# Optimization experiments

Measured on AMD Instinct MI355X. Metric: run time of the kernel, lower is better.

## Reference

```python
import jax, jax.numpy as jnp
import numpy as np

WL = 8  # word length passed to block_quantize_nearest


def block_quantize_nearest(x, wl=WL):
    """QPyTorch block_quantize_nearest with dim=0.

    One shared exponent per row (block = row of x.view(N, -1)).
    Equivalent math to the CUDA kernel: base exponent e = floor(log2(max|row|)),
    quantization step = 2^(e + 2 - wl), round-half-up in the rebased bit space.
    """
    flat = x.reshape(x.shape[0], -1)
    max_abs = jnp.max(jnp.abs(flat), axis=1, keepdims=True)  # [N, 1]
    tiny = jnp.asarray(np.finfo(np.float32).tiny, x.dtype)
    exp = jnp.floor(jnp.log2(jnp.maximum(max_abs, tiny)))
    step = jnp.exp2(exp + 2.0 - wl)                          # [N, 1]
    q = jnp.floor(flat / step + 0.5) * step                  # round-half-up
    q = jnp.where(max_abs > 0, q, flat)                      # all-zero rows pass through
    return q.reshape(x.shape)


def setup_inputs() -> dict:
    key = jax.random.key(0)
    k1, k2, k3 = jax.random.split(key, 3)
    B, D_IN, D_OUT = 8192, 4096, 4096
    x = jax.random.normal(k1, (B, D_IN), dtype=jnp.float32)
    # nn.Linear init scale ~ 1/sqrt(fan_in)
    W = jax.random.normal(k2, (D_OUT, D_IN), dtype=jnp.float32) * (1.0 / np.sqrt(D_IN))
    b = jax.random.normal(k3, (D_OUT,), dtype=jnp.float32) * (1.0 / np.sqrt(D_IN))
    return {"x": x, "W": W, "b": b}


def reference(x, W, b):
    # Linear: y = x @ W^T + b  (x already 2D, flatten(1) is identity)
    h = jnp.einsum('bi,oi->bo', x.reshape(x.shape[0], -1), W) + b
    q = block_quantize_nearest(h, WL)
    return jax.nn.relu(q)
```

## Files before the change

kernel.cpp:

```cpp
#include <hip/hip_runtime.h>

#define M 8192
#define N 4096
#define K 4096
#define BM 256
#define BN 256
#define BK 64
#define NKT (K / BK)
#define NIT (NKT / 2)

typedef __attribute__((ext_vector_type(8))) short bf16x8;
typedef __attribute__((ext_vector_type(4))) float f32x4;
typedef __attribute__((address_space(1))) const unsigned GU;
typedef __attribute__((address_space(3))) unsigned LU;

__device__ __forceinline__ unsigned short f2bf(float f) {
    unsigned u = __float_as_uint(f);
    u += 0x7fffu + ((u >> 16) & 1u);
    return (unsigned short)(u >> 16);
}

__global__ __launch_bounds__(256) void cvt_bf16(const float* __restrict__ src,
                                                unsigned short* __restrict__ dst,
                                                int n8) {
    const int stride = gridDim.x * blockDim.x;
    for (int i = blockIdx.x * blockDim.x + threadIdx.x; i < n8; i += stride) {
        f32x4 a = ((const f32x4*)src)[2 * i];
        f32x4 b = ((const f32x4*)src)[2 * i + 1];
        bf16x8 v;
        #pragma unroll
        for (int j = 0; j < 4; ++j) {
            v[j]     = (short)f2bf(a[j]);
            v[4 + j] = (short)f2bf(b[j]);
        }
        ((bf16x8*)dst)[i] = v;
    }
}

#define BAR()   __builtin_amdgcn_s_barrier()
#define LGKM0() do { asm volatile("s_waitcnt lgkmcnt(0)" ::: "memory"); \
                     __builtin_amdgcn_sched_barrier(0); } while (0)
#define LGKM8() asm volatile("s_waitcnt lgkmcnt(8)" ::: "memory")
#define VM6()   asm volatile("s_waitcnt vmcnt(6)" ::: "memory")

#define QUAD(AR, BR, MOFF, NOFF)                                               \
    do {                                                                       \
        __builtin_amdgcn_s_setprio(1);                                         \
        _Pragma("unroll")                                                      \
        for (int m_ = 0; m_ < 4; ++m_) {                                       \
            _Pragma("unroll")                                                  \
            for (int n_ = 0; n_ < 2; ++n_) {                                   \
                acc[MOFF + m_][NOFF + n_] =                                    \
                    __builtin_amdgcn_mfma_f32_16x16x32_bf16(                   \
                        AR[m_][0], BR[n_][0], acc[MOFF + m_][NOFF + n_], 0, 0, 0); \
                acc[MOFF + m_][NOFF + n_] =                                    \
                    __builtin_amdgcn_mfma_f32_16x16x32_bf16(                   \
                        AR[m_][1], BR[n_][1], acc[MOFF + m_][NOFF + n_], 0, 0, 0); \
            }                                                                  \
        }                                                                      \
        __builtin_amdgcn_s_setprio(0);                                         \
    } while (0)

__global__ __launch_bounds__(512, 2) void gemm_bf16(
    const unsigned short* __restrict__ xb, const unsigned short* __restrict__ wb,
    const float* __restrict__ bias, float* __restrict__ out,
    int* __restrict__ rowmax)
{
    __shared__ short As[2][16384];
    __shared__ short Bs[2][16384];

    const int bid = blockIdx.x;
    const int tm = bid % (M / BM);
    const int tn = bid / (M / BM);
    const int bm = tm * BM, bn = tn * BN;

    const int t    = threadIdx.x;
    const int w_id = t >> 6;
    const int l    = t & 63;
    const int wr   = w_id >> 2;
    const int wc   = w_id & 3;
    const int lr   = l & 15;
    const int g    = l >> 4;

    const int srow_l = l >> 2;
    const int scol_l = ((l & 3) * 8) ^ ((l >> 5) * 16);
    const int loff = lr * 32 + ((g * 8) ^ ((lr >> 3) << 4));

    auto stageA = [&](int buf, int h, int kt) {
        #pragma unroll
        for (int j = 0; j < 2; ++j) {
            const int s = w_id * 2 + j;
            const unsigned short* gp =
                xb + (size_t)(bm + h * 128 + (s >> 1) * 16 + srow_l) * K
                   + kt * 64 + (s & 1) * 32 + scol_l;
            __builtin_amdgcn_global_load_lds(
                (const GU*)gp, (LU*)&As[buf][h * 8192 + s * 512], 16, 0, 0);
        }
    };
    auto stageB = [&](int buf, int h, int kt) {
        #pragma unroll
        for (int j = 0; j < 2; ++j) {
            const int s = w_id * 2 + j;
            const unsigned short* gp =
                wb + (size_t)(bn + h * 128 + (s >> 1) * 16 + srow_l) * K
                   + kt * 64 + (s & 1) * 32 + scol_l;
            __builtin_amdgcn_global_load_lds(
                (const GU*)gp, (LU*)&Bs[buf][h * 8192 + s * 512], 16, 0, 0);
        }
    };
    auto ldA = [&](int buf, int m, int ks) -> bf16x8 {
        return *(const bf16x8*)&As[buf][wr * 8192 + (m * 2 + ks) * 512 + loff];
    };
    auto ldB = [&](int buf, int n, int ks) -> bf16x8 {
        return *(const bf16x8*)&Bs[buf][(wc >> 1) * 8192 +
                                        (((wc & 1) * 4 + n) * 2 + ks) * 512 + loff];
    };

    f32x4 acc[8][4];
    #pragma unroll
    for (int m = 0; m < 8; ++m)
        #pragma unroll
        for (int n = 0; n < 4; ++n)
            acc[m][n] = (f32x4){0.f, 0.f, 0.f, 0.f};

    bf16x8 a03[4][2], a47[4][2], b01[2][2], b23[2][2];

    stageB(0, 0, 0); stageB(0, 1, 0); stageA(0, 0, 0); stageA(0, 1, 0);
    stageB(1, 0, 1); stageB(1, 1, 1); stageA(1, 0, 1);
    VM6();
    BAR();

    for (int it = 0; it < NIT; ++it) {
        const int t1  = 2 * it + 1;
        const int tp0 = (2 * it + 2) & (NKT - 1);
        const int tp1 = (2 * it + 3) & (NKT - 1);

        #pragma unroll
        for (int m = 0; m < 4; ++m) { a03[m][0] = ldA(0, m, 0); a03[m][1] = ldA(0, m, 1); }
        #pragma unroll
        for (int n = 0; n < 2; ++n) { b01[n][0] = ldB(0, n, 0); b01[n][1] = ldB(0, n, 1); }
        stageA(1, 1, t1);
        LGKM8();
        BAR(); LGKM0();
        QUAD(a03, b01, 0, 0);
        BAR();

        #pragma unroll
        for (int n = 0; n < 2; ++n) { b23[n][0] = ldB(0, 2 + n, 0); b23[n][1] = ldB(0, 2 + n, 1); }
        stageB(0, 0, tp0);
        BAR(); LGKM0();
        QUAD(a03, b23, 0, 2);
        BAR();

        #pragma unroll
        for (int m = 0; m < 4; ++m) { a47[m][0] = ldA(0, 4 + m, 0); a47[m][1] = ldA(0, 4 + m, 1); }
        stageB(0, 1, tp0);
        BAR(); LGKM0();
        QUAD(a47, b23, 4, 2);
        BAR();

        stageA(0, 0, tp0);
        BAR(); LGKM0();
        QUAD(a47, b01, 4, 0);
        VM6();
        BAR();

        #pragma unroll
        for (int m = 0; m < 4; ++m) { a03[m][0] = ldA(1, m, 0); a03[m][1] = ldA(1, m, 1); }
        #pragma unroll
        for (int n = 0; n < 2; ++n) { b01[n][0] = ldB(1, n, 0); b01[n][1] = ldB(1, n, 1); }
        stageA(0, 1, tp0);
        LGKM8();
        BAR(); LGKM0();
        QUAD(a03, b01, 0, 0);
        BAR();

        #pragma unroll
        for (int n = 0; n < 2; ++n) { b23[n][0] = ldB(1, 2 + n, 0); b23[n][1] = ldB(1, 2 + n, 1); }
        stageB(1, 0, tp1);
        BAR(); LGKM0();
        QUAD(a03, b23, 0, 2);
        BAR();

        #pragma unroll
        for (int m = 0; m < 4; ++m) { a47[m][0] = ldA(1, 4 + m, 0); a47[m][1] = ldA(1, 4 + m, 1); }
        stageB(1, 1, tp1);
        BAR(); LGKM0();
        QUAD(a47, b23, 4, 2);
        BAR();

        stageA(1, 0, tp1);
        BAR(); LGKM0();
        QUAD(a47, b01, 4, 0);
        VM6();
        BAR();
    }

    float bv[4];
    #pragma unroll
    for (int n = 0; n < 4; ++n)
        bv[n] = bias[bn + wc * 64 + n * 16 + lr];

    #pragma unroll
    for (int m = 0; m < 8; ++m) {
        #pragma unroll
        for (int r = 0; r < 4; ++r) {
            const int row = bm + wr * 128 + m * 16 + g * 4 + r;
            float amax = 0.f;
            #pragma unroll
            for (int n = 0; n < 4; ++n) {
                const float v = acc[m][n][r] + bv[n];
                out[(size_t)row * N + (bn + wc * 64 + n * 16 + lr)] = v;
                amax = fmaxf(amax, fabsf(v));
            }
            #pragma unroll
            for (int off = 1; off < 16; off <<= 1)
                amax = fmaxf(amax, __shfl_xor(amax, off));
            if (lr == 0)
                atomicMax(rowmax + row, __float_as_int(amax));
        }
    }
}

__global__ __launch_bounds__(256) void quant_relu(
    float* __restrict__ y, const int* __restrict__ rowmax)
{
    const int nvec = (M * N) / 4;
    for (int i = blockIdx.x * blockDim.x + threadIdx.x; i < nvec;
         i += gridDim.x * blockDim.x) {
        const int row = i >> 10;
        const float mx = __int_as_float(rowmax[row]);
        f32x4 v = ((const f32x4*)y)[i];
        if (mx > 0.f) {
            const int e = ilogbf(mx);
            const float step = ldexpf(1.0f, e - 6);
            const float inv  = ldexpf(1.0f, 6 - e);
            #pragma unroll
            for (int j = 0; j < 4; ++j)
                v[j] = floorf(v[j] * inv + 0.5f) * step;
        }
        #pragma unroll
        for (int j = 0; j < 4; ++j)
            v[j] = fmaxf(v[j], 0.f);
        ((f32x4*)y)[i] = v;
    }
}

extern "C" void kernel_launch(void* const* d_in, const int* in_sizes, int n_in,
                              void* d_out, int out_size, void* d_ws, size_t ws_size,
                              hipStream_t stream) {
    const float* x = (const float*)d_in[0];
    const float* w = (const float*)d_in[1];
    const float* b = (const float*)d_in[2];
    float* out = (float*)d_out;

    const size_t XB = (size_t)M * K * 2;
    const size_t WB = (size_t)N * K * 2;

    unsigned short* xb = (unsigned short*)d_ws;
    unsigned short* wb = (unsigned short*)((char*)d_ws + XB);
    int* rowmax        = (int*)((char*)d_ws + XB + WB);

    hipMemsetAsync(rowmax, 0, M * sizeof(int), stream);
    cvt_bf16<<<2048, 256, 0, stream>>>(x, xb, (M * K) / 8);
    cvt_bf16<<<1024, 256, 0, stream>>>(w, wb, (N * K) / 8);
    gemm_bf16<<<dim3((M / BM) * (N / BN)), 512, 0, stream>>>(xb, wb, b, out, rowmax);
    quant_relu<<<2048, 256, 0, stream>>>(out, rowmax);
}
```

Baseline: 546.0 us.

## Stage GEMM epilogue through LDS for coalesced stores and fuse cvt kernels

The GEMM epilogue now writes the biased accumulators into the reused LDS buffer, one 128-row half at a time, and then issues fully coalesced 16-byte row-contiguous stores to the output. Previously each lane wrote scattered 4-byte values. The two bf16 conversion launches are also merged into one kernel that processes 4 elements per thread, saving one launch. The cost is extra barriers and an LDS round trip in the epilogue, and the conversion kernel now does narrower per-thread work.

Measured after the change: 534.9 us. 2.0% less time.

```diff
diff --git a/kernel.cpp b/kernel.cpp
--- a/kernel.cpp
+++ b/kernel.cpp
@@ -10,6 +10,7 @@
 #define NIT (NKT / 2)
 
 typedef __attribute__((ext_vector_type(8))) short bf16x8;
+typedef __attribute__((ext_vector_type(4))) short bf16x4;
 typedef __attribute__((ext_vector_type(4))) float f32x4;
 typedef __attribute__((address_space(1))) const unsigned GU;
 typedef __attribute__((address_space(3))) unsigned LU;
@@ -20,20 +21,23 @@
     return (unsigned short)(u >> 16);
 }
 
-__global__ __launch_bounds__(256) void cvt_bf16(const float* __restrict__ src,
-                                                unsigned short* __restrict__ dst,
-                                                int n8) {
+__global__ __launch_bounds__(256) void cvt_bf16_2(
+    const float* __restrict__ s1, unsigned short* __restrict__ d1, int n1_4,
+    const float* __restrict__ s2, unsigned short* __restrict__ d2, int n2_4)
+{
     const int stride = gridDim.x * blockDim.x;
-    for (int i = blockIdx.x * blockDim.x + threadIdx.x; i < n8; i += stride) {
-        f32x4 a = ((const f32x4*)src)[2 * i];
-        f32x4 b = ((const f32x4*)src)[2 * i + 1];
-        bf16x8 v;
-        #pragma unroll
-        for (int j = 0; j < 4; ++j) {
-            v[j]     = (short)f2bf(a[j]);
-            v[4 + j] = (short)f2bf(b[j]);
-        }
-        ((bf16x8*)dst)[i] = v;
+    const int total = n1_4 + n2_4;
+    for (int i = blockIdx.x * blockDim.x + threadIdx.x; i < total; i += stride) {
+        const float* s;
+        unsigned short* d;
+        int j;
+        if (i < n1_4) { s = s1; d = d1; j = i; }
+        else          { s = s2; d = d2; j = i - n1_4; }
+        f32x4 v = ((const f32x4*)s)[j];
+        bf16x4 o;
+        #pragma unroll
+        for (int k = 0; k < 4; ++k) o[k] = (short)f2bf(v[k]);
+        ((bf16x4*)d)[j] = o;
     }
 }
 
@@ -66,8 +70,7 @@
     const float* __restrict__ bias, float* __restrict__ out,
     int* __restrict__ rowmax)
 {
-    __shared__ short As[2][16384];
-    __shared__ short Bs[2][16384];
+    __shared__ __align__(16) short smem[65536];
 
     const int bid = blockIdx.x;
     const int tm = bid % (M / BM);
@@ -94,7 +97,7 @@
                 xb + (size_t)(bm + h * 128 + (s >> 1) * 16 + srow_l) * K
                    + kt * 64 + (s & 1) * 32 + scol_l;
             __builtin_amdgcn_global_load_lds(
-                (const GU*)gp, (LU*)&As[buf][h * 8192 + s * 512], 16, 0, 0);
+                (const GU*)gp, (LU*)&smem[buf * 16384 + h * 8192 + s * 512], 16, 0, 0);
         }
     };
     auto stageB = [&](int buf, int h, int kt) {
@@ -105,15 +108,15 @@
                 wb + (size_t)(bn + h * 128 + (s >> 1) * 16 + srow_l) * K
                    + kt * 64 + (s & 1) * 32 + scol_l;
             __builtin_amdgcn_global_load_lds(
-                (const GU*)gp, (LU*)&Bs[buf][h * 8192 + s * 512], 16, 0, 0);
+                (const GU*)gp, (LU*)&smem[32768 + buf * 16384 + h * 8192 + s * 512], 16, 0, 0);
         }
     };
     auto ldA = [&](int buf, int m, int ks) -> bf16x8 {
-        return *(const bf16x8*)&As[buf][wr * 8192 + (m * 2 + ks) * 512 + loff];
+        return *(const bf16x8*)&smem[buf * 16384 + wr * 8192 + (m * 2 + ks) * 512 + loff];
     };
     auto ldB = [&](int buf, int n, int ks) -> bf16x8 {
-        return *(const bf16x8*)&Bs[buf][(wc >> 1) * 8192 +
-                                        (((wc & 1) * 4 + n) * 2 + ks) * 512 + loff];
+        return *(const bf16x8*)&smem[32768 + buf * 16384 + (wc >> 1) * 8192 +
+                                     (((wc & 1) * 4 + n) * 2 + ks) * 512 + loff];
     };
 
     f32x4 acc[8][4];
@@ -196,6 +199,8 @@
         BAR();
     }
 
+    __syncthreads();
+
     float bv[4];
     #pragma unroll
     for (int n = 0; n < 4; ++n)
@@ -209,15 +214,39 @@
             float amax = 0.f;
             #pragma unroll
             for (int n = 0; n < 4; ++n) {
-                const float v = acc[m][n][r] + bv[n];
-                out[(size_t)row * N + (bn + wc * 64 + n * 16 + lr)] = v;
-                amax = fmaxf(amax, fabsf(v));
+                acc[m][n][r] += bv[n];
+                amax = fmaxf(amax, fabsf(acc[m][n][r]));
             }
             #pragma unroll
             for (int off = 1; off < 16; off <<= 1)
                 amax = fmaxf(amax, __shfl_xor(amax, off));
             if (lr == 0)
                 atomicMax(rowmax + row, __float_as_int(amax));
+        }
+    }
+
+    float* hs = (float*)smem;
+    #pragma unroll
+    for (int p = 0; p < 2; ++p) {
+        if (p) __syncthreads();
+        if (wr == p) {
+            #pragma unroll
+            for (int m = 0; m < 8; ++m)
+                #pragma unroll
+                for (int r = 0; r < 4; ++r)
+                    #pragma unroll
+                    for (int n = 0; n < 4; ++n)
+                        hs[(m * 16 + g * 4 + r) * 256 + wc * 64 + n * 16 + lr] =
+                            acc[m][n][r];
+        }
+        __syncthreads();
+        #pragma unroll
+        for (int j = 0; j < 16; ++j) {
+            const int fi  = j * 2048 + t * 4;
+            const int row = fi >> 8;
+            const int col = fi & 255;
+            *(f32x4*)&out[(size_t)(bm + p * 128 + row) * N + bn + col] =
+                *(const f32x4*)&hs[fi];
         }
     }
 }
@@ -262,8 +291,7 @@
     int* rowmax        = (int*)((char*)d_ws + XB + WB);
 
     hipMemsetAsync(rowmax, 0, M * sizeof(int), stream);
-    cvt_bf16<<<2048, 256, 0, stream>>>(x, xb, (M * K) / 8);
-    cvt_bf16<<<1024, 256, 0, stream>>>(w, wb, (N * K) / 8);
+    cvt_bf16_2<<<3072, 256, 0, stream>>>(x, xb, (M * K) / 4, w, wb, (N * K) / 4);
     gemm_bf16<<<dim3((M / BM) * (N / BN)), 512, 0, stream>>>(xb, wb, b, out, rowmax);
     quant_relu<<<2048, 256, 0, stream>>>(out, rowmax);
 }
```
